# Kernel tuning notes

Measured on AMD Instinct MI355X. Metric: run time of the kernel, lower is better.

Reference implementation:

```python
import jax, jax.numpy as jnp
import numpy as np

N_HEAD = 8
D_ATTN = 64
D_MODEL = 512


def setup_inputs() -> dict:
    key = jax.random.key(0)
    ks = jax.random.split(key, 12)
    B, S = 2, 2048
    inp = {
        "input": jax.random.normal(ks[0], (B, S, D_MODEL), dtype=jnp.float32),
        "top": jax.random.normal(ks[1], (B, S, S, 16), dtype=jnp.float32),
        # learned params (Linear: y = x @ W.T + b)
        "top_w": jax.random.normal(ks[2], (1, 16), dtype=jnp.float32) * 0.25,
        "top_b": jnp.zeros((1,), dtype=jnp.float32),
        "wq": jax.random.normal(ks[3], (N_HEAD * D_ATTN, D_MODEL), dtype=jnp.float32) * 0.02,
        "bq": jnp.zeros((N_HEAD * D_ATTN,), dtype=jnp.float32),
        "wk": jax.random.normal(ks[4], (N_HEAD * D_ATTN, D_MODEL), dtype=jnp.float32) * 0.02,
        "bk": jnp.zeros((N_HEAD * D_ATTN,), dtype=jnp.float32),
        "wv": jax.random.normal(ks[5], (N_HEAD * D_ATTN, D_MODEL), dtype=jnp.float32) * 0.02,
        "bv": jnp.zeros((N_HEAD * D_ATTN,), dtype=jnp.float32),
        "wo": jax.random.normal(ks[6], (D_MODEL, N_HEAD * D_ATTN), dtype=jnp.float32) * 0.02,
        "bo": jnp.zeros((D_MODEL,), dtype=jnp.float32),
    }
    return inp


def reference(input, top, top_w, top_b, wq, bq, wk, bk, wv, bv, wo, bo):
    B, S, _ = input.shape
    # pairwise topological bias: [B,S,S,16] @ [16,1] -> [B,S,S]
    bias = (jnp.einsum('bstf,f->bst', top, top_w[0]) + top_b[0])  # [B,S,S]
    bias = bias[:, None, :, :]  # broadcast over heads: [B,1,S,S]

    def proj(w, b):
        # [B,S,D] -> [B,H,S,d]
        return (input @ w.T + b).reshape(B, S, N_HEAD, D_ATTN).transpose(0, 2, 1, 3)

    Q, K, V = proj(wq, bq), proj(wk, bk), proj(wv, bv)
    scores = jnp.einsum('bhqd,bhkd->bhqk', Q, K) / jnp.sqrt(jnp.float32(D_ATTN))
    attn = jax.nn.softmax(scores + bias, axis=-1)
    O = jnp.einsum('bhqk,bhkd->bhqd', attn, V)  # [B,H,S,d]
    O = O.transpose(0, 2, 1, 3).reshape(B, S, N_HEAD * D_ATTN)
    return O @ wo.T + bo
```

## Files before the change

### kernel.cpp

```cpp
#include <hip/hip_runtime.h>
#include <math.h>

#define S_LEN 2048
#define BATCH 2
#define NH 8
#define DH 64
#define DM 512

typedef __attribute__((ext_vector_type(8))) short short8;
typedef __attribute__((ext_vector_type(4))) float floatx4;

__device__ __forceinline__ unsigned short f2bf(float f) {
  union { float f; unsigned u; } v; v.f = f;
  unsigned r = v.u + 0x7FFFu + ((v.u >> 16) & 1u);
  return (unsigned short)(r >> 16);
}

__global__ __launch_bounds__(256) void cvt_f32_bf16(const float* __restrict__ src,
                                                    unsigned short* __restrict__ dst, int n4) {
  int i = blockIdx.x * blockDim.x + threadIdx.x;
  if (i < n4) {
    float4 f = ((const float4*)src)[i];
    ushort4 o;
    o.x = f2bf(f.x); o.y = f2bf(f.y); o.z = f2bf(f.z); o.w = f2bf(f.w);
    ((ushort4*)dst)[i] = o;
  }
}

__global__ __launch_bounds__(256) void cvt4_f32_bf16(const float* __restrict__ a, const float* __restrict__ b,
                                                     const float* __restrict__ c, const float* __restrict__ d,
                                                     unsigned short* __restrict__ oa, unsigned short* __restrict__ ob,
                                                     unsigned short* __restrict__ oc, unsigned short* __restrict__ od) {
  const float* src; unsigned short* dst;
  switch (blockIdx.y) {
    case 0: src = a; dst = oa; break;
    case 1: src = b; dst = ob; break;
    case 2: src = c; dst = oc; break;
    default: src = d; dst = od; break;
  }
  int i = blockIdx.x * blockDim.x + threadIdx.x;
  float4 f = ((const float4*)src)[i];
  ushort4 o;
  o.x = f2bf(f.x); o.y = f2bf(f.y); o.z = f2bf(f.z); o.w = f2bf(f.w);
  ((ushort4*)dst)[i] = o;
}

__global__ __launch_bounds__(256) void bias_topo(const float* __restrict__ top,
                                                 const float* __restrict__ top_w,
                                                 const float* __restrict__ top_b,
                                                 float* __restrict__ bias) {
  size_t e = (size_t)blockIdx.x * blockDim.x + threadIdx.x;
  const float4* t = (const float4*)(top + e * 16);
  const float4* w = (const float4*)top_w;
  float acc = top_b[0];
#pragma unroll
  for (int j = 0; j < 4; j++) {
    float4 tv = t[j]; float4 wv = w[j];
    acc += tv.x * wv.x + tv.y * wv.y + tv.z * wv.z + tv.w * wv.w;
  }
  bias[e] = acc;
}

__global__ __launch_bounds__(256) void gemm_bt(const unsigned short* __restrict__ A,
                                               const unsigned short* __restrict__ W,
                                               const float* __restrict__ bias,
                                               void* __restrict__ out, int mode, float scale) {
  __shared__ unsigned short As[64][72];
  __shared__ unsigned short Ws[64][72];
  const int m0 = blockIdx.x * 64, n0 = blockIdx.y * 64;
  const int tid = threadIdx.x;
  const int w = tid >> 6, l = tid & 63;
  const int lr = l & 15, lg = l >> 4;

  floatx4 acc[4];
#pragma unroll
  for (int nb = 0; nb < 4; nb++)
#pragma unroll
    for (int i = 0; i < 4; i++) acc[nb][i] = 0.f;

  const int srow = tid >> 2;
  const int sseg = (tid & 3) * 16;

  for (int k0 = 0; k0 < 512; k0 += 64) {
    const unsigned short* ap = A + (size_t)(m0 + srow) * 512 + k0 + sseg;
    const unsigned short* wp = W + (size_t)(n0 + srow) * 512 + k0 + sseg;
    *(short8*)&As[srow][sseg]     = *(const short8*)ap;
    *(short8*)&As[srow][sseg + 8] = *(const short8*)(ap + 8);
    *(short8*)&Ws[srow][sseg]     = *(const short8*)wp;
    *(short8*)&Ws[srow][sseg + 8] = *(const short8*)(wp + 8);
    __syncthreads();
#pragma unroll
    for (int kk = 0; kk < 2; kk++) {
      short8 af = *(const short8*)&As[w * 16 + lr][kk * 32 + lg * 8];
#pragma unroll
      for (int nb = 0; nb < 4; nb++) {
        short8 bf = *(const short8*)&Ws[nb * 16 + lr][kk * 32 + lg * 8];
        acc[nb] = __builtin_amdgcn_mfma_f32_16x16x32_bf16(af, bf, acc[nb], 0, 0, 0);
      }
    }
    __syncthreads();
  }

  if (mode == 2) {
#pragma unroll
    for (int nb = 0; nb < 4; nb++) {
      const float bv = bias[n0 + nb * 16 + lr];
      ushort4 pk;
      pk.x = f2bf(acc[nb][0] + bv);
      pk.y = f2bf(acc[nb][1] + bv);
      pk.z = f2bf(acc[nb][2] + bv);
      pk.w = f2bf(acc[nb][3] + bv);
      *(ushort4*)&As[nb * 16 + lr][w * 16 + lg * 4] = pk;
    }
    __syncthreads();
    const int b = m0 >> 11, s_base = m0 & 2047;
    const int h = n0 >> 6;
    unsigned short* outp = (unsigned short*)out + (size_t)(b * 8 + h) * DH * S_LEN;
    const int row = tid >> 2, seg = (tid & 3) * 16;
    short8 v0 = *(const short8*)&As[row][seg];
    short8 v1 = *(const short8*)&As[row][seg + 8];
    *(short8*)(outp + (size_t)row * S_LEN + s_base + seg)     = v0;
    *(short8*)(outp + (size_t)row * S_LEN + s_base + seg + 8) = v1;
    return;
  }

#pragma unroll
  for (int nb = 0; nb < 4; nb++) {
    const int n = n0 + nb * 16 + lr;
    const float bv = bias[n];
#pragma unroll
    for (int i = 0; i < 4; i++) {
      const int m = m0 + w * 16 + lg * 4 + i;
      float v = (acc[nb][i] + bv) * scale;
      if (mode == 0) {
        ((float*)out)[(size_t)m * 512 + n] = v;
      } else {
        const int b = m >> 11, s = m & 2047;
        const int h = n >> 6, d = n & 63;
        ((unsigned short*)out)[((size_t)(b * 8 + h) * 2048 + s) * 64 + d] = f2bf(v);
      }
    }
  }
}

__global__ __launch_bounds__(256) void attn_kernel(const unsigned short* __restrict__ Qb,
                                                   const unsigned short* __restrict__ Kb,
                                                   const unsigned short* __restrict__ Vt,
                                                   const float* __restrict__ biasb,
                                                   unsigned short* __restrict__ Ob) {
  __shared__ unsigned short Ps[4][16][72];
  const int q0 = blockIdx.x * 64;
  const int bh = blockIdx.y;
  const int b = bh >> 3, h = bh & 7;
  const int tid = threadIdx.x;
  const int w = tid >> 6, l = tid & 63;
  const int lr = l & 15, lg = l >> 4;

  const unsigned short* Qh = Qb + (size_t)bh * S_LEN * DH;
  const unsigned short* Kh = Kb + (size_t)bh * S_LEN * DH;
  const unsigned short* Vh = Vt + (size_t)bh * DH * S_LEN;

  const int q = q0 + w * 16 + lr;
  short8 qf[2];
  qf[0] = *(const short8*)(Qh + (size_t)q * DH + lg * 8);
  qf[1] = *(const short8*)(Qh + (size_t)q * DH + 32 + lg * 8);

  float m_i = -1e30f, l_i = 0.f;
  floatx4 o[4];
#pragma unroll
  for (int nd = 0; nd < 4; nd++)
#pragma unroll
    for (int i = 0; i < 4; i++) o[nd][i] = 0.f;

  const float* brow = biasb + ((size_t)b * S_LEN + q) * S_LEN;
  const float LOG2E = 1.44269504088896f;

  for (int k0 = 0; k0 < S_LEN; k0 += 64) {
    floatx4 sa[4];
#pragma unroll
    for (int nb = 0; nb < 4; nb++)
#pragma unroll
      for (int i = 0; i < 4; i++) sa[nb][i] = 0.f;
#pragma unroll
    for (int kk = 0; kk < 2; kk++) {
#pragma unroll
      for (int nb = 0; nb < 4; nb++) {
        short8 kf = *(const short8*)(Kh + (size_t)(k0 + nb * 16 + lr) * DH + kk * 32 + lg * 8);
        sa[nb] = __builtin_amdgcn_mfma_f32_16x16x32_bf16(kf, qf[kk], sa[nb], 0, 0, 0);
      }
    }
    float p[4][4];
    float mx = -1e30f;
#pragma unroll
    for (int nb = 0; nb < 4; nb++) {
      float4 bv = *(const float4*)(brow + k0 + nb * 16 + lg * 4);
      p[nb][0] = sa[nb][0] + bv.x;
      p[nb][1] = sa[nb][1] + bv.y;
      p[nb][2] = sa[nb][2] + bv.z;
      p[nb][3] = sa[nb][3] + bv.w;
      mx = fmaxf(mx, fmaxf(fmaxf(p[nb][0], p[nb][1]), fmaxf(p[nb][2], p[nb][3])));
    }
    mx = fmaxf(mx, __shfl_xor(mx, 16));
    mx = fmaxf(mx, __shfl_xor(mx, 32));
    const float mnew = fmaxf(m_i, mx);
    const float alpha = exp2f((m_i - mnew) * LOG2E);
    float rs = 0.f;
#pragma unroll
    for (int nb = 0; nb < 4; nb++)
#pragma unroll
      for (int i = 0; i < 4; i++) {
        p[nb][i] = exp2f((p[nb][i] - mnew) * LOG2E);
        rs += p[nb][i];
      }
    rs += __shfl_xor(rs, 16);
    rs += __shfl_xor(rs, 32);
    l_i = l_i * alpha + rs;
    m_i = mnew;
#pragma unroll
    for (int nd = 0; nd < 4; nd++)
#pragma unroll
      for (int i = 0; i < 4; i++) o[nd][i] *= alpha;
#pragma unroll
    for (int nb = 0; nb < 4; nb++) {
      ushort4 pk;
      pk.x = f2bf(p[nb][0]); pk.y = f2bf(p[nb][1]);
      pk.z = f2bf(p[nb][2]); pk.w = f2bf(p[nb][3]);
      *(ushort4*)&Ps[w][lr][nb * 16 + lg * 4] = pk;
    }
#pragma unroll
    for (int kk = 0; kk < 2; kk++) {
      short8 pf = *(const short8*)&Ps[w][lr][kk * 32 + lg * 8];
#pragma unroll
      for (int nd = 0; nd < 4; nd++) {
        short8 vf = *(const short8*)(Vh + (size_t)(nd * 16 + lr) * S_LEN + k0 + kk * 32 + lg * 8);
        o[nd] = __builtin_amdgcn_mfma_f32_16x16x32_bf16(vf, pf, o[nd], 0, 0, 0);
      }
    }
  }

  const float inv = 1.0f / l_i;
#pragma unroll
  for (int nd = 0; nd < 4; nd++) {
    ushort4 st;
    st.x = f2bf(o[nd][0] * inv);
    st.y = f2bf(o[nd][1] * inv);
    st.z = f2bf(o[nd][2] * inv);
    st.w = f2bf(o[nd][3] * inv);
    *(ushort4*)(Ob + ((size_t)b * S_LEN + q) * DM + h * DH + nd * 16 + lg * 4) = st;
  }
}

extern "C" void kernel_launch(void* const* d_in, const int* in_sizes, int n_in,
                              void* d_out, int out_size, void* d_ws, size_t ws_size,
                              hipStream_t stream) {
  const float* input = (const float*)d_in[0];
  const float* top   = (const float*)d_in[1];
  const float* top_w = (const float*)d_in[2];
  const float* top_b = (const float*)d_in[3];
  const float* wq = (const float*)d_in[4];
  const float* bq = (const float*)d_in[5];
  const float* wk = (const float*)d_in[6];
  const float* bk = (const float*)d_in[7];
  const float* wv = (const float*)d_in[8];
  const float* bv = (const float*)d_in[9];
  const float* wo = (const float*)d_in[10];
  const float* bo = (const float*)d_in[11];

  char* ws = (char*)d_ws;
  float* bias_ws = (float*)ws;              ws += (size_t)BATCH * S_LEN * S_LEN * 4;
  unsigned short* in_bf = (unsigned short*)ws;  ws += (size_t)BATCH * S_LEN * DM * 2;
  unsigned short* wq_bf = (unsigned short*)ws;  ws += (size_t)DM * DM * 2;
  unsigned short* wk_bf = (unsigned short*)ws;  ws += (size_t)DM * DM * 2;
  unsigned short* wv_bf = (unsigned short*)ws;  ws += (size_t)DM * DM * 2;
  unsigned short* wo_bf = (unsigned short*)ws;  ws += (size_t)DM * DM * 2;
  unsigned short* qb  = (unsigned short*)ws;    ws += (size_t)BATCH * NH * S_LEN * DH * 2;
  unsigned short* kb  = (unsigned short*)ws;    ws += (size_t)BATCH * NH * S_LEN * DH * 2;
  unsigned short* vtb = (unsigned short*)ws;    ws += (size_t)BATCH * NH * S_LEN * DH * 2;
  unsigned short* ob  = (unsigned short*)ws;    ws += (size_t)BATCH * S_LEN * DM * 2;

  const int nIn4 = BATCH * S_LEN * DM / 4;
  const int nW4  = DM * DM / 4;
  cvt_f32_bf16<<<nIn4 / 256, 256, 0, stream>>>(input, in_bf, nIn4);
  cvt4_f32_bf16<<<dim3(nW4 / 256, 4), 256, 0, stream>>>(wq, wk, wv, wo, wq_bf, wk_bf, wv_bf, wo_bf);

  bias_topo<<<(BATCH * S_LEN * S_LEN) / 256, 256, 0, stream>>>(top, top_w, top_b, bias_ws);

  dim3 gg(4096 / 64, 512 / 64);
  gemm_bt<<<gg, 256, 0, stream>>>(in_bf, wq_bf, bq, qb, 1, 0.125f);
  gemm_bt<<<gg, 256, 0, stream>>>(in_bf, wk_bf, bk, kb, 1, 1.0f);
  gemm_bt<<<gg, 256, 0, stream>>>(in_bf, wv_bf, bv, vtb, 2, 1.0f);

  attn_kernel<<<dim3(S_LEN / 64, BATCH * NH), 256, 0, stream>>>(qb, kb, vtb, bias_ws, ob);

  gemm_bt<<<gg, 256, 0, stream>>>(ob, wo_bf, bo, d_out, 0, 1.0f);
}
```

Measured before the change: 894.6 us.

## Fuse conversion and QKV launches, fold log2e into scores and bias

Merges the input and weight bf16 conversions into one kernel and the three Q/K/V projection GEMMs into one launch indexed by blockIdx.z. Pre-multiplies the topological bias and the Q scale by log2(e), so the softmax can call exp2 directly without an extra multiply. Replaces manual bf16 rounding with the packed hardware conversion intrinsic. The intent is to cut launch overhead and per-element ALU work in attention. The gemm now does per-block pointer selection.

Result: no change. 878.4 us (-1.8%).

```diff
diff --git a/kernel.cpp b/kernel.cpp
--- a/kernel.cpp
+++ b/kernel.cpp
@@ -1,4 +1,5 @@
 #include <hip/hip_runtime.h>
+#include <hip/hip_bf16.h>
 #include <math.h>
 
 #define S_LEN 2048
@@ -6,6 +7,7 @@
 #define NH 8
 #define DH 64
 #define DM 512
+#define LOG2E 1.44269504088896f
 
 typedef __attribute__((ext_vector_type(8))) short short8;
 typedef __attribute__((ext_vector_type(4))) float floatx4;
@@ -16,33 +18,34 @@
   return (unsigned short)(r >> 16);
 }
 
-__global__ __launch_bounds__(256) void cvt_f32_bf16(const float* __restrict__ src,
-                                                    unsigned short* __restrict__ dst, int n4) {
-  int i = blockIdx.x * blockDim.x + threadIdx.x;
-  if (i < n4) {
-    float4 f = ((const float4*)src)[i];
-    ushort4 o;
-    o.x = f2bf(f.x); o.y = f2bf(f.y); o.z = f2bf(f.z); o.w = f2bf(f.w);
-    ((ushort4*)dst)[i] = o;
-  }
-}
-
-__global__ __launch_bounds__(256) void cvt4_f32_bf16(const float* __restrict__ a, const float* __restrict__ b,
-                                                     const float* __restrict__ c, const float* __restrict__ d,
-                                                     unsigned short* __restrict__ oa, unsigned short* __restrict__ ob,
-                                                     unsigned short* __restrict__ oc, unsigned short* __restrict__ od) {
-  const float* src; unsigned short* dst;
-  switch (blockIdx.y) {
-    case 0: src = a; dst = oa; break;
-    case 1: src = b; dst = ob; break;
-    case 2: src = c; dst = oc; break;
-    default: src = d; dst = od; break;
-  }
-  int i = blockIdx.x * blockDim.x + threadIdx.x;
+__device__ __forceinline__ unsigned pkbf(float a, float b) {
+  __hip_bfloat162 h = __float22bfloat162_rn(make_float2(a, b));
+  union { __hip_bfloat162 h; unsigned u; } v; v.h = h;
+  return v.u;
+}
+
+__global__ __launch_bounds__(256) void cvt_all(const float* __restrict__ in,
+                                               const float* __restrict__ wq, const float* __restrict__ wk,
+                                               const float* __restrict__ wv, const float* __restrict__ wo,
+                                               unsigned short* __restrict__ in_bf,
+                                               unsigned short* __restrict__ qw, unsigned short* __restrict__ kw,
+                                               unsigned short* __restrict__ vw, unsigned short* __restrict__ ow) {
+  int bid = blockIdx.x;
+  const float* src; unsigned short* dst; int base;
+  if (bid < 2048) { src = in; dst = in_bf; base = bid; }
+  else {
+    int wsel = (bid - 2048) >> 8;
+    base = (bid - 2048) & 255;
+    switch (wsel) {
+      case 0: src = wq; dst = qw; break;
+      case 1: src = wk; dst = kw; break;
+      case 2: src = wv; dst = vw; break;
+      default: src = wo; dst = ow; break;
+    }
+  }
+  int i = base * 256 + threadIdx.x;
   float4 f = ((const float4*)src)[i];
-  ushort4 o;
-  o.x = f2bf(f.x); o.y = f2bf(f.y); o.z = f2bf(f.z); o.w = f2bf(f.w);
-  ((ushort4*)dst)[i] = o;
+  ((uint2*)dst)[i] = make_uint2(pkbf(f.x, f.y), pkbf(f.z, f.w));
 }
 
 __global__ __launch_bounds__(256) void bias_topo(const float* __restrict__ top,
@@ -58,15 +61,26 @@
     float4 tv = t[j]; float4 wv = w[j];
     acc += tv.x * wv.x + tv.y * wv.y + tv.z * wv.z + tv.w * wv.w;
   }
-  bias[e] = acc;
+  bias[e] = acc * LOG2E;
 }
 
 __global__ __launch_bounds__(256) void gemm_bt(const unsigned short* __restrict__ A,
-                                               const unsigned short* __restrict__ W,
-                                               const float* __restrict__ bias,
-                                               void* __restrict__ out, int mode, float scale) {
+                                               const unsigned short* __restrict__ W0,
+                                               const unsigned short* __restrict__ W1,
+                                               const unsigned short* __restrict__ W2,
+                                               const float* __restrict__ b0, const float* __restrict__ b1,
+                                               const float* __restrict__ b2,
+                                               void* __restrict__ o0, void* __restrict__ o1, void* __restrict__ o2,
+                                               int qkv, float scale0) {
   __shared__ unsigned short As[64][72];
   __shared__ unsigned short Ws[64][72];
+  const int z = qkv ? blockIdx.z : 0;
+  const unsigned short* W = (z == 0) ? W0 : (z == 1) ? W1 : W2;
+  const float* bias = (z == 0) ? b0 : (z == 1) ? b1 : b2;
+  void* out = (z == 0) ? o0 : (z == 1) ? o1 : o2;
+  const int mode = qkv ? ((z == 2) ? 2 : 1) : 0;
+  const float scale = (z == 0) ? scale0 : 1.0f;
+
   const int m0 = blockIdx.x * 64, n0 = blockIdx.y * 64;
   const int tid = threadIdx.x;
   const int w = tid >> 6, l = tid & 63;
@@ -105,12 +119,9 @@
 #pragma unroll
     for (int nb = 0; nb < 4; nb++) {
       const float bv = bias[n0 + nb * 16 + lr];
-      ushort4 pk;
-      pk.x = f2bf(acc[nb][0] + bv);
-      pk.y = f2bf(acc[nb][1] + bv);
-      pk.z = f2bf(acc[nb][2] + bv);
-      pk.w = f2bf(acc[nb][3] + bv);
-      *(ushort4*)&As[nb * 16 + lr][w * 16 + lg * 4] = pk;
+      unsigned lo = pkbf(acc[nb][0] + bv, acc[nb][1] + bv);
+      unsigned hi = pkbf(acc[nb][2] + bv, acc[nb][3] + bv);
+      *(uint2*)&As[nb * 16 + lr][w * 16 + lg * 4] = make_uint2(lo, hi);
     }
     __syncthreads();
     const int b = m0 >> 11, s_base = m0 & 2047;
@@ -173,7 +184,6 @@
     for (int i = 0; i < 4; i++) o[nd][i] = 0.f;
 
   const float* brow = biasb + ((size_t)b * S_LEN + q) * S_LEN;
-  const float LOG2E = 1.44269504088896f;
 
   for (int k0 = 0; k0 < S_LEN; k0 += 64) {
     floatx4 sa[4];
@@ -203,13 +213,13 @@
     mx = fmaxf(mx, __shfl_xor(mx, 16));
     mx = fmaxf(mx, __shfl_xor(mx, 32));
     const float mnew = fmaxf(m_i, mx);
-    const float alpha = exp2f((m_i - mnew) * LOG2E);
+    const float alpha = exp2f(m_i - mnew);
     float rs = 0.f;
 #pragma unroll
     for (int nb = 0; nb < 4; nb++)
 #pragma unroll
       for (int i = 0; i < 4; i++) {
-        p[nb][i] = exp2f((p[nb][i] - mnew) * LOG2E);
+        p[nb][i] = exp2f(p[nb][i] - mnew);
         rs += p[nb][i];
       }
     rs += __shfl_xor(rs, 16);
@@ -222,10 +232,9 @@
       for (int i = 0; i < 4; i++) o[nd][i] *= alpha;
 #pragma unroll
     for (int nb = 0; nb < 4; nb++) {
-      ushort4 pk;
-      pk.x = f2bf(p[nb][0]); pk.y = f2bf(p[nb][1]);
-      pk.z = f2bf(p[nb][2]); pk.w = f2bf(p[nb][3]);
-      *(ushort4*)&Ps[w][lr][nb * 16 + lg * 4] = pk;
+      unsigned lo = pkbf(p[nb][0], p[nb][1]);
+      unsigned hi = pkbf(p[nb][2], p[nb][3]);
+      *(uint2*)&Ps[w][lr][nb * 16 + lg * 4] = make_uint2(lo, hi);
     }
 #pragma unroll
     for (int kk = 0; kk < 2; kk++) {
@@ -241,12 +250,9 @@
   const float inv = 1.0f / l_i;
 #pragma unroll
   for (int nd = 0; nd < 4; nd++) {
-    ushort4 st;
-    st.x = f2bf(o[nd][0] * inv);
-    st.y = f2bf(o[nd][1] * inv);
-    st.z = f2bf(o[nd][2] * inv);
-    st.w = f2bf(o[nd][3] * inv);
-    *(ushort4*)(Ob + ((size_t)b * S_LEN + q) * DM + h * DH + nd * 16 + lg * 4) = st;
+    unsigned lo = pkbf(o[nd][0] * inv, o[nd][1] * inv);
+    unsigned hi = pkbf(o[nd][2] * inv, o[nd][3] * inv);
+    *(uint2*)(Ob + ((size_t)b * S_LEN + q) * DM + h * DH + nd * 16 + lg * 4) = make_uint2(lo, hi);
   }
 }
 
@@ -278,19 +284,15 @@
   unsigned short* vtb = (unsigned short*)ws;    ws += (size_t)BATCH * NH * S_LEN * DH * 2;
   unsigned short* ob  = (unsigned short*)ws;    ws += (size_t)BATCH * S_LEN * DM * 2;
 
-  const int nIn4 = BATCH * S_LEN * DM / 4;
-  const int nW4  = DM * DM / 4;
-  cvt_f32_bf16<<<nIn4 / 256, 256, 0, stream>>>(input, in_bf, nIn4);
-  cvt4_f32_bf16<<<dim3(nW4 / 256, 4), 256, 0, stream>>>(wq, wk, wv, wo, wq_bf, wk_bf, wv_bf, wo_bf);
+  cvt_all<<<3072, 256, 0, stream>>>(input, wq, wk, wv, wo, in_bf, wq_bf, wk_bf, wv_bf, wo_bf);
 
   bias_topo<<<(BATCH * S_LEN * S_LEN) / 256, 256, 0, stream>>>(top, top_w, top_b, bias_ws);
 
-  dim3 gg(4096 / 64, 512 / 64);
-  gemm_bt<<<gg, 256, 0, stream>>>(in_bf, wq_bf, bq, qb, 1, 0.125f);
-  gemm_bt<<<gg, 256, 0, stream>>>(in_bf, wk_bf, bk, kb, 1, 1.0f);
-  gemm_bt<<<gg, 256, 0, stream>>>(in_bf, wv_bf, bv, vtb, 2, 1.0f);
+  gemm_bt<<<dim3(4096 / 64, 512 / 64, 3), 256, 0, stream>>>(
+      in_bf, wq_bf, wk_bf, wv_bf, bq, bk, bv, qb, kb, vtb, 1, 0.125f * LOG2E);
 
   attn_kernel<<<dim3(S_LEN / 64, BATCH * NH), 256, 0, stream>>>(qb, kb, vtb, bias_ws, ob);
 
-  gemm_bt<<<gg, 256, 0, stream>>>(ob, wo_bf, bo, d_out, 0, 1.0f);
-}
+  gemm_bt<<<dim3(4096 / 64, 512 / 64, 1), 256, 0, stream>>>(
+      ob, wo_bf, nullptr, nullptr, bo, nullptr, nullptr, d_out, nullptr, nullptr, 0, 1.0f);
+}
```
